# Kernel optimization log

Measured on AMD Instinct MI355X. Metric: run time of the kernel, lower is better.

## Reference

```python
import jax, jax.numpy as jnp
import numpy as np

B, T, C = 2, 2048, 1024
N_HEAD, N_GROUP = 16, 4
N_KV = N_HEAD // N_GROUP          # 4
HEAD_DIM = C // N_HEAD            # 64
ROPE_BASE = 10000.0
INIT_STD = 0.02


def setup_inputs() -> dict:
    key = jax.random.key(0)
    ks = jax.random.split(key, 5)
    kvC = N_KV * HEAD_DIM
    return {
        "x": jax.random.normal(ks[0], (B, T, C), jnp.float32),
        "w_q": jax.random.normal(ks[1], (C, C), jnp.float32) * INIT_STD,
        "b_q": jnp.zeros((C,), jnp.float32),
        "w_k": jax.random.normal(ks[2], (C, kvC), jnp.float32) * INIT_STD,
        "b_k": jnp.zeros((kvC,), jnp.float32),
        "w_v": jax.random.normal(ks[3], (C, kvC), jnp.float32) * INIT_STD,
        "b_v": jnp.zeros((kvC,), jnp.float32),
        "w_o": jax.random.normal(ks[4], (C, C), jnp.float32) * INIT_STD,
        "b_o": jnp.zeros((C,), jnp.float32),
    }


def reference(x, w_q, b_q, w_k, b_k, w_v, b_v, w_o, b_o):
    Bx, Tx, Cx = x.shape
    # projections (torch Linear math with weights stored as [in, out])
    q = (x @ w_q + b_q).reshape(Bx, Tx, N_HEAD, HEAD_DIM).transpose(0, 2, 1, 3)  # [B,H,T,hd]
    k = (x @ w_k + b_k).reshape(Bx, Tx, N_KV, HEAD_DIM).transpose(0, 2, 1, 3)    # [B,KV,T,hd]
    v = (x @ w_v + b_v).reshape(Bx, Tx, N_KV, HEAD_DIM).transpose(0, 2, 1, 3)

    # RoPE with INTERLEAVED pair convention: pairs are (dim 2i, dim 2i+1)
    inv_freq = 1.0 / (ROPE_BASE ** (jnp.arange(0, HEAD_DIM, 2, dtype=jnp.float32) / HEAD_DIM))
    freqs = jnp.arange(Tx, dtype=jnp.float32)[:, None] * inv_freq[None, :]       # [T, hd/2]
    cos, sin = jnp.cos(freqs), jnp.sin(freqs)

    def rope(t):
        tp = t.reshape(*t.shape[:-1], HEAD_DIM // 2, 2)
        e, o = tp[..., 0], tp[..., 1]          # even/odd lanes, [B,h,T,hd/2]
        er = e * cos - o * sin
        orr = e * sin + o * cos
        return jnp.stack([er, orr], axis=-1).reshape(t.shape)

    q, k = rope(q), rope(k)

    # GQA: duplicate each KV head n_group times (consecutively, like repeat_interleave)
    k = jnp.repeat(k, N_GROUP, axis=1)   # [B,H,T,hd]
    v = jnp.repeat(v, N_GROUP, axis=1)

    attn = jnp.einsum('bhqd,bhkd->bhqk', q, k) / np.sqrt(HEAD_DIM).astype(np.float32)
    causal = jnp.tril(jnp.ones((Tx, Tx), bool))
    attn = jnp.where(causal, attn, -jnp.inf)
    attn = jax.nn.softmax(attn, axis=-1)

    out = jnp.einsum('bhqk,bhkd->bhqd', attn, v)            # [B,H,T,hd]
    out = out.transpose(0, 2, 1, 3).reshape(Bx, Tx, Cx)
    return out @ w_o + b_o
```

## Files before the change

### kernel.cpp

```cpp
#include <hip/hip_runtime.h>
#include <hip/hip_bf16.h>

typedef __hip_bfloat16 bf16;
typedef __attribute__((ext_vector_type(8))) short short8_t;
typedef __attribute__((ext_vector_type(4))) short short4_t;
typedef __attribute__((ext_vector_type(4))) float f32x4;

#define B_SZ   2
#define T_SEQ  2048
#define C_DIM  1024
#define NH     16
#define NKV    4
#define HD     64
#define QKVW   1536
#define MTOK   (B_SZ * T_SEQ)

#define LOG2_BASE_OVER_32 0.4152410118609203f
#define Q_SCALE 0.1803368801111204f

__device__ __forceinline__ short f2bs(float f) {
    unsigned u = __float_as_uint(f);
    u += 0x7FFFu + ((u >> 16) & 1u);
    return (short)(u >> 16);
}
__device__ __forceinline__ short f2bs_trunc(float f) {
    return (short)(__float_as_uint(f) >> 16);
}
__device__ __forceinline__ float bs2f(short s) {
    unsigned u = ((unsigned)(unsigned short)s) << 16;
    return __uint_as_float(u);
}
__device__ __forceinline__ float dpp_xor1(float x) {
    return __int_as_float(
        __builtin_amdgcn_update_dpp(0, __float_as_int(x), 0xB1, 0xF, 0xF, true));
}
__device__ __forceinline__ float fast_exp2(float x) {
    float r;
    asm("v_exp_f32 %0, %1" : "=v"(r) : "v"(x));
    return r;
}
__device__ __forceinline__ unsigned pack_bf16_trunc(float lo, float hi) {
    return __builtin_amdgcn_perm(__float_as_uint(hi), __float_as_uint(lo),
                                 0x07060302u);
}
__device__ __forceinline__ void gload_lds16(const short* g, short* l) {
    __builtin_amdgcn_global_load_lds(
        (const __attribute__((address_space(1))) void*)g,
        (__attribute__((address_space(3))) void*)l, 16, 0, 0);
}

__device__ __forceinline__ void transpose_tile(
    const float* __restrict__ W, short* __restrict__ Wt,
    int K, int N, int n0, int k0, int tid)
{
    __shared__ float tile[32][33];
    int tx = tid & 31, ty = tid >> 5;
    #pragma unroll
    for (int i = 0; i < 4; ++i)
        tile[ty + 8 * i][tx] = W[(size_t)(k0 + ty + 8 * i) * N + n0 + tx];
    __syncthreads();
    #pragma unroll
    for (int i = 0; i < 4; ++i)
        Wt[(size_t)(n0 + ty + 8 * i) * K + k0 + tx] = f2bs(tile[tx][ty + 8 * i]);
}

__global__ __launch_bounds__(256) void prep_kernel(
    const float* __restrict__ x,
    const float* __restrict__ w_q, const float* __restrict__ w_k,
    const float* __restrict__ w_v, const float* __restrict__ w_o,
    const float* __restrict__ b_q, const float* __restrict__ b_k,
    const float* __restrict__ b_v,
    short* __restrict__ Xb, short* __restrict__ Wqkv, short* __restrict__ Wto,
    float* __restrict__ Bqkv, float2* __restrict__ Tab)
{
    int blk = blockIdx.x, tid = threadIdx.x;
    if (blk < 4096) {
        int i = blk * 1024 + tid * 4;
        float4 v = *(const float4*)(x + i);
        short4_t o;
        o[0] = f2bs(v.x); o[1] = f2bs(v.y); o[2] = f2bs(v.z); o[3] = f2bs(v.w);
        *(short4_t*)(Xb + i) = o;
    } else if (blk < 5120) {
        int l = blk - 4096;
        transpose_tile(w_q, Wqkv, C_DIM, C_DIM, (l & 31) * 32, (l >> 5) * 32, tid);
    } else if (blk < 5376) {
        int l = blk - 5120;
        transpose_tile(w_k, Wqkv + (size_t)1024 * C_DIM, C_DIM, 256,
                       (l & 7) * 32, (l >> 3) * 32, tid);
    } else if (blk < 5632) {
        int l = blk - 5376;
        transpose_tile(w_v, Wqkv + (size_t)1280 * C_DIM, C_DIM, 256,
                       (l & 7) * 32, (l >> 3) * 32, tid);
    } else if (blk < 6656) {
        int l = blk - 5632;
        transpose_tile(w_o, Wto, C_DIM, C_DIM, (l & 31) * 32, (l >> 5) * 32, tid);
    } else if (blk < 6662) {
        int i = (blk - 6656) * 256 + tid;
        float v;
        if (i < 1024)      v = b_q[i];
        else if (i < 1280) v = b_k[i - 1024];
        else               v = b_v[i - 1280];
        Bqkv[i] = v;
    } else {
        int idx = (blk - 6662) * 256 + tid;
        int t = idx >> 5, i = idx & 31;
        float ang = (float)t * exp2f(-(float)i * LOG2_BASE_OVER_32);
        Tab[idx] = make_float2(cosf(ang), sinf(ang));
    }
}

#define GEMM_STAGE(dstA, dstB, Aptr, Bptr, k0)                                  \
    {                                                                           \
        _Pragma("unroll")                                                       \
        for (int it = 0; it < 4; ++it) {                                        \
            int i = (w * 4 + it) * 64 + lane;                                   \
            int row = i >> 3, p = i & 7;                                        \
            int gc = (k0) + ((p ^ (row & 7)) << 3);                             \
            gload_lds16((Aptr) + (size_t)(m0 + row) * K + gc,                   \
                        (dstA) + (w * 4 + it) * 512);                           \
        }                                                                       \
        _Pragma("unroll")                                                       \
        for (int it = 0; it < 4; ++it) {                                        \
            int i = (w * 4 + it) * 64 + lane;                                   \
            int row = i >> 3, p = i & 7;                                        \
            int gc = (k0) + ((p ^ (row & 7)) << 3);                             \
            gload_lds16((Bptr) + (size_t)(n0 + row) * K + gc,                   \
                        (dstB) + (w * 4 + it) * 512);                           \
        }                                                                       \
    }

#define GEMM_COMPUTE(srcA, srcB)                                                \
    {                                                                           \
        _Pragma("unroll")                                                       \
        for (int ks = 0; ks < 2; ++ks) {                                        \
            short8_t af[4], bf[4];                                              \
            _Pragma("unroll")                                                   \
            for (int mt = 0; mt < 4; ++mt) {                                    \
                int r = wm * 64 + mt * 16 + l16;                                \
                int g = ks * 4 + quad;                                          \
                af[mt] = *(const short8_t*)&(srcA)[r * 64 + ((g ^ (r & 7)) << 3)]; \
            }                                                                   \
            _Pragma("unroll")                                                   \
            for (int nt = 0; nt < 4; ++nt) {                                    \
                int r = wn * 64 + nt * 16 + l16;                                \
                int g = ks * 4 + quad;                                          \
                bf[nt] = *(const short8_t*)&(srcB)[r * 64 + ((g ^ (r & 7)) << 3)]; \
            }                                                                   \
            _Pragma("unroll")                                                   \
            for (int mt = 0; mt < 4; ++mt)                                      \
                _Pragma("unroll")                                               \
                for (int nt = 0; nt < 4; ++nt)                                  \
                    acc[mt][nt] = __builtin_amdgcn_mfma_f32_16x16x32_bf16(      \
                        af[mt], bf[nt], acc[mt][nt], 0, 0, 0);                  \
        }                                                                       \
    }

#define GEMM_KLOOP(Aptr, Bptr)                                                  \
    GEMM_STAGE(sA(0), sB(0), Aptr, Bptr, 0);                                    \
    for (int t = 0; t < NT; ++t) {                                              \
        int cur = t & 1;                                                        \
        if (t + 1 < NT) {                                                       \
            GEMM_STAGE(sA(cur ^ 1), sB(cur ^ 1), Aptr, Bptr, (t + 1) * 64);     \
            asm volatile("s_waitcnt vmcnt(8)" ::: "memory");                    \
        } else {                                                                \
            asm volatile("s_waitcnt vmcnt(0)" ::: "memory");                    \
        }                                                                       \
        __builtin_amdgcn_s_barrier();                                           \
        __builtin_amdgcn_sched_barrier(0);                                      \
        GEMM_COMPUTE(sA(cur), sB(cur));                                         \
        __builtin_amdgcn_sched_barrier(0);                                      \
        __builtin_amdgcn_s_barrier();                                           \
    }

__global__ __launch_bounds__(256) void gemm_qkv(
    const short* __restrict__ A, const short* __restrict__ Bt,
    const float* __restrict__ bias, const float2* __restrict__ Tab,
    short* __restrict__ QKVb, short* __restrict__ Vt)
{
    __shared__ __align__(16) short smem[32768];
    #define sA(b) (smem + (b) * 16384)
    #define sB(b) (smem + (b) * 16384 + 8192)

    const int K = C_DIM, NT = C_DIM / 64;
    int m0 = blockIdx.y * 128;
    int n0 = blockIdx.x * 128;
    int tid  = threadIdx.x;
    int w    = tid >> 6, lane = tid & 63;
    int quad = lane >> 4, l16 = lane & 15;
    int wm = w & 1, wn = w >> 1;

    f32x4 acc[4][4] = {};

    GEMM_KLOOP(A, Bt);

    if (n0 < 1280) {
        float scale = (n0 < 1024) ? Q_SCALE : 1.0f;
        float sgn   = (l16 & 1) ? 1.0f : -1.0f;
        #pragma unroll
        for (int nt = 0; nt < 4; ++nt) {
            int col = n0 + wn * 64 + nt * 16 + l16;
            int ip  = (col & 63) >> 1;
            float bv = bias[col];
            #pragma unroll
            for (int mt = 0; mt < 4; ++mt) {
                #pragma unroll
                for (int r = 0; r < 4; ++r) {
                    int row = m0 + wm * 64 + mt * 16 + quad * 4 + r;
                    float v = acc[mt][nt][r] + bv;
                    float po = dpp_xor1(v);
                    float2 cs = Tab[(row & (T_SEQ - 1)) * 32 + ip];
                    float res = (v * cs.x + sgn * po * cs.y) * scale;
                    QKVb[(size_t)row * QKVW + col] = f2bs(res);
                }
            }
        }
    } else {
        short (*sT)[136] = (short(*)[136])smem;
        #pragma unroll
        for (int h2 = 0; h2 < 2; ++h2) {
            if (wn == h2) {
                #pragma unroll
                for (int nt = 0; nt < 4; ++nt) {
                    int col_l = nt * 16 + l16;
                    float bv = bias[n0 + h2 * 64 + col_l];
                    #pragma unroll
                    for (int mt = 0; mt < 4; ++mt)
                        #pragma unroll
                        for (int r = 0; r < 4; ++r)
                            sT[col_l][wm * 64 + mt * 16 + quad * 4 + r] =
                                f2bs(acc[mt][nt][r] + bv);
                }
            }
            __syncthreads();
            int d0 = n0 - 1280 + h2 * 64;
            #pragma unroll
            for (int it = 0; it < 4; ++it) {
                int slot = tid + 256 * it;
                int dl = slot >> 4, seg = (slot & 15) * 8;
                *(short8_t*)(Vt + (size_t)(d0 + dl) * MTOK + m0 + seg) =
                    *(const short8_t*)&sT[dl][seg];
            }
            __syncthreads();
        }
    }
    #undef sA
    #undef sB
}

__global__ __launch_bounds__(256) void gemm_mfma_o(
    const short* __restrict__ A, const short* __restrict__ Bt,
    const float* __restrict__ bias, float* __restrict__ C,
    int M, int N, int K_, int unused)
{
    __shared__ __align__(16) short smem[32768];
    #define sA(b) (smem + (b) * 16384)
    #define sB(b) (smem + (b) * 16384 + 8192)

    const int K = C_DIM, NT = C_DIM / 64;
    int m0 = blockIdx.y * 128;
    int n0 = blockIdx.x * 128;
    int tid  = threadIdx.x;
    int w    = tid >> 6, lane = tid & 63;
    int quad = lane >> 4, l16 = lane & 15;
    int wm = w & 1, wn = w >> 1;

    f32x4 acc[4][4] = {};

    GEMM_KLOOP(A, Bt);

    #pragma unroll
    for (int mt = 0; mt < 4; ++mt) {
        #pragma unroll
        for (int nt = 0; nt < 4; ++nt) {
            int col = n0 + wn * 64 + nt * 16 + l16;
            float bv = bias[col];
            #pragma unroll
            for (int r = 0; r < 4; ++r) {
                int row = m0 + wm * 64 + mt * 16 + quad * 4 + r;
                C[(size_t)row * N + col] = acc[mt][nt][r] + bv;
            }
        }
    }
    #undef sA
    #undef sB
}

__global__ __launch_bounds__(256) void attn_mfma11(
    const short* __restrict__ QKV, const short* __restrict__ Vt,
    short* __restrict__ O)
{
    __shared__ __align__(16) short sK [2][64][72];
    __shared__ __align__(16) short sVt[2][64][72];

    const int tid  = threadIdx.x;
    const int w    = tid >> 6;
    const int lane = tid & 63;
    const int quad = lane >> 4;
    const int l16  = lane & 15;

    int blk = blockIdx.x;
    int grp = blk & 7;
    int tq  = 127 - (blk >> 3);
    int kvh = grp & 3;
    int b   = grp >> 2;
    int h   = kvh * 4 + w;
    int ct  = tq >> 2;
    int tg  = tq * 16 + l16;

    const short* qptr = QKV + ((size_t)(b * T_SEQ) + tq * 16 + l16) * QKVW + h * HD;
    short8_t qf0 = *(const short8_t*)(qptr + quad * 8);
    short8_t qf1 = *(const short8_t*)(qptr + quad * 8 + 32);

    const short* kbase  = QKV + (size_t)b * T_SEQ * QKVW + 1024 + kvh * HD;
    const short* vtbase = Vt + (size_t)(kvh * HD) * MTOK + b * T_SEQ;

    float m_l = -INFINITY, l_l = 0.f;
    f32x4 oacc[4];
    #pragma unroll
    for (int dt = 0; dt < 4; ++dt) oacc[dt] = (f32x4){0.f, 0.f, 0.f, 0.f};

    const int kkey = tid >> 3, kd = (tid & 7) * 8;
    const int vdim = tid >> 3;
    const int s8   = tid & 7;
    const int vseg = s8 * 8;
    const int P0 = ((s8 & 4) << 3) | ((s8 & 1) << 4) | ((s8 & 2) << 1);

    short8_t kr[2], vr[2];
    #pragma unroll
    for (int it = 0; it < 2; ++it) {
        kr[it] = *(const short8_t*)(kbase + (size_t)(kkey + 32 * it) * QKVW + kd);
        vr[it] = *(const short8_t*)(vtbase + (size_t)(vdim + 32 * it) * MTOK + vseg);
    }

    #pragma unroll
    for (int it = 0; it < 2; ++it) {
        *(short8_t*)&sK[0][kkey + 32 * it][kd] = kr[it];
        union { short8_t v; short4_t h[2]; } u; u.v = vr[it];
        *(short4_t*)&sVt[0][vdim + 32 * it][P0]     = u.h[0];
        *(short4_t*)&sVt[0][vdim + 32 * it][P0 + 8] = u.h[1];
    }
    __syncthreads();

    for (int c = 0; c <= ct; ++c) {
        const int buf = c & 1;

        if (c < ct) {
            int jn = (c + 1) * 64;
            #pragma unroll
            for (int it = 0; it < 2; ++it) {
                kr[it] = *(const short8_t*)(kbase + (size_t)(jn + kkey + 32 * it) * QKVW + kd);
                vr[it] = *(const short8_t*)(vtbase + (size_t)(vdim + 32 * it) * MTOK + jn + vseg);
            }
        }

        f32x4 sacc[4];
        __builtin_amdgcn_s_setprio(1);
        #pragma unroll
        for (int kt = 0; kt < 4; ++kt) {
            f32x4 z = {0.f, 0.f, 0.f, 0.f};
            short8_t kf0 = *(const short8_t*)&sK[buf][l16 + 16 * kt][quad * 8];
            short8_t kf1 = *(const short8_t*)&sK[buf][l16 + 16 * kt][quad * 8 + 32];
            z = __builtin_amdgcn_mfma_f32_16x16x32_bf16(kf0, qf0, z, 0, 0, 0);
            z = __builtin_amdgcn_mfma_f32_16x16x32_bf16(kf1, qf1, z, 0, 0, 0);
            sacc[kt] = z;
        }
        __builtin_amdgcn_s_setprio(0);

        short8_t vf0[4];
        #pragma unroll
        for (int dt = 0; dt < 4; ++dt)
            vf0[dt] = *(const short8_t*)&sVt[buf][16 * dt + l16][quad * 8];

        if (c == ct) {
            int j0 = c * 64;
            #pragma unroll
            for (int kt = 0; kt < 4; ++kt)
                #pragma unroll
                for (int r = 0; r < 4; ++r)
                    if (j0 + 16 * kt + quad * 4 + r > tg) sacc[kt][r] = -INFINITY;
        }

        float v0 = fmaxf(fmaxf(sacc[0][0], sacc[0][1]), fmaxf(sacc[0][2], sacc[0][3]));
        float v1 = fmaxf(fmaxf(sacc[1][0], sacc[1][1]), fmaxf(sacc[1][2], sacc[1][3]));
        float v2 = fmaxf(fmaxf(sacc[2][0], sacc[2][1]), fmaxf(sacc[2][2], sacc[2][3]));
        float v3 = fmaxf(fmaxf(sacc[3][0], sacc[3][1]), fmaxf(sacc[3][2], sacc[3][3]));
        float vloc = fmaxf(fmaxf(v0, v1), fmaxf(v2, v3));

        if (!__all(vloc <= m_l + 8.0f)) {
            float vmax = fmaxf(vloc, __shfl_xor(vloc, 16));
            vmax = fmaxf(vmax, __shfl_xor(vmax, 32));
            float mnew = fmaxf(m_l, vmax);
            float al = fast_exp2(m_l - mnew);
            m_l = mnew;
            l_l *= al;
            #pragma unroll
            for (int r = 0; r < 4; ++r) {
                float alr = __shfl(al, quad * 4 + r);
                #pragma unroll
                for (int dt = 0; dt < 4; ++dt) oacc[dt][r] *= alr;
            }
        }

        float psum = 0.f;
        unsigned pk0, pk1, pk2, pk3, pk4, pk5, pk6, pk7;
        {
            float p0 = fast_exp2(sacc[0][0] - m_l), p1 = fast_exp2(sacc[0][1] - m_l);
            float p2 = fast_exp2(sacc[0][2] - m_l), p3 = fast_exp2(sacc[0][3] - m_l);
            psum += (p0 + p1) + (p2 + p3);
            pk0 = pack_bf16_trunc(p0, p1); pk1 = pack_bf16_trunc(p2, p3);
        }
        {
            float p0 = fast_exp2(sacc[1][0] - m_l), p1 = fast_exp2(sacc[1][1] - m_l);
            float p2 = fast_exp2(sacc[1][2] - m_l), p3 = fast_exp2(sacc[1][3] - m_l);
            psum += (p0 + p1) + (p2 + p3);
            pk2 = pack_bf16_trunc(p0, p1); pk3 = pack_bf16_trunc(p2, p3);
        }
        {
            float p0 = fast_exp2(sacc[2][0] - m_l), p1 = fast_exp2(sacc[2][1] - m_l);
            float p2 = fast_exp2(sacc[2][2] - m_l), p3 = fast_exp2(sacc[2][3] - m_l);
            psum += (p0 + p1) + (p2 + p3);
            pk4 = pack_bf16_trunc(p0, p1); pk5 = pack_bf16_trunc(p2, p3);
        }
        {
            float p0 = fast_exp2(sacc[3][0] - m_l), p1 = fast_exp2(sacc[3][1] - m_l);
            float p2 = fast_exp2(sacc[3][2] - m_l), p3 = fast_exp2(sacc[3][3] - m_l);
            psum += (p0 + p1) + (p2 + p3);
            pk6 = pack_bf16_trunc(p0, p1); pk7 = pack_bf16_trunc(p2, p3);
        }
        l_l += psum;

        short8_t pf0, pf1;
        {
            union { unsigned u[4]; short8_t v; } fa, fb;
            fa.u[0] = pk0; fa.u[1] = pk1; fa.u[2] = pk2; fa.u[3] = pk3;
            fb.u[0] = pk4; fb.u[1] = pk5; fb.u[2] = pk6; fb.u[3] = pk7;
            pf0 = fa.v; pf1 = fb.v;
        }

        __builtin_amdgcn_s_setprio(1);
        #pragma unroll
        for (int dt = 0; dt < 4; ++dt) {
            short8_t vf1 = *(const short8_t*)&sVt[buf][16 * dt + l16][quad * 8 + 32];
            oacc[dt] = __builtin_amdgcn_mfma_f32_16x16x32_bf16(pf0, vf0[dt], oacc[dt], 0, 0, 0);
            oacc[dt] = __builtin_amdgcn_mfma_f32_16x16x32_bf16(pf1, vf1, oacc[dt], 0, 0, 0);
        }
        __builtin_amdgcn_s_setprio(0);

        if (c < ct) {
            #pragma unroll
            for (int it = 0; it < 2; ++it) {
                *(short8_t*)&sK[buf ^ 1][kkey + 32 * it][kd] = kr[it];
                union { short8_t v; short4_t h[2]; } u; u.v = vr[it];
                *(short4_t*)&sVt[buf ^ 1][vdim + 32 * it][P0]     = u.h[0];
                *(short4_t*)&sVt[buf ^ 1][vdim + 32 * it][P0 + 8] = u.h[1];
            }
        }
        __syncthreads();
    }

    l_l += __shfl_xor(l_l, 16);
    l_l += __shfl_xor(l_l, 32);

    #pragma unroll
    for (int r = 0; r < 4; ++r) {
        int m = quad * 4 + r;
        float lr = __shfl(l_l, quad * 4 + r);
        float inv = __builtin_amdgcn_rcpf(lr);
        #pragma unroll
        for (int dt = 0; dt < 4; ++dt)
            O[((size_t)b * T_SEQ + tq * 16 + m) * C_DIM + h * HD + 16 * dt + l16] =
                f2bs(oacc[dt][r] * inv);
    }
}

extern "C" void kernel_launch(void* const* d_in, const int* in_sizes, int n_in,
                              void* d_out, int out_size, void* d_ws, size_t ws_size,
                              hipStream_t stream)
{
    const float* x   = (const float*)d_in[0];
    const float* w_q = (const float*)d_in[1];
    const float* b_q = (const float*)d_in[2];
    const float* w_k = (const float*)d_in[3];
    const float* b_k = (const float*)d_in[4];
    const float* w_v = (const float*)d_in[5];
    const float* b_v = (const float*)d_in[6];
    const float* w_o = (const float*)d_in[7];
    const float* b_o = (const float*)d_in[8];
    float* out = (float*)d_out;

    char* ws = (char*)d_ws;
    short*  Xb   = (short*) (ws);
    short*  Ab   = (short*) (ws + ((size_t)8  << 20));
    short*  QKVb = (short*) (ws + ((size_t)16 << 20));
    short*  Wqkv = (short*) (ws + ((size_t)28 << 20));
    short*  Wto  = (short*) (ws + ((size_t)31 << 20));
    float*  Bqkv = (float*) (ws + ((size_t)33 << 20));
    float2* Tab  = (float2*)(ws + ((size_t)33 << 20) + 8192);
    short*  Vt   = (short*) (ws + ((size_t)34 << 20));

    const int M = MTOK;

    prep_kernel<<<6918, 256, 0, stream>>>(
        x, w_q, w_k, w_v, w_o, b_q, b_k, b_v, Xb, Wqkv, Wto, Bqkv, Tab);

    gemm_qkv<<<dim3(QKVW / 128, M / 128), 256, 0, stream>>>(
        Xb, Wqkv, Bqkv, Tab, QKVb, Vt);

    attn_mfma11<<<B_SZ * NKV * 128, 256, 0, stream>>>(QKVb, Vt, Ab);

    gemm_mfma_o<<<dim3(C_DIM / 128, M / 128), 256, 0, stream>>>(
        Ab, Wto, b_o, out, M, C_DIM, C_DIM, 0);
}
```

Baseline: 164.6 us.

## Share K/V tiles across two query tiles per 512-thread attention block

The attention kernel now runs 512 threads (8 waves) per block, covering two adjacent 16-row query tiles for the four heads of a KV group. Each loaded K/V tile is therefore reused by twice as many waves, and the grid is halved. K is moved into LDS with direct global-to-LDS loads (gload_lds16) into an XOR-swizzled, unpadded layout, replacing the register staging. Risks are lower occupancy from the larger blocks, more waves waiting at each barrier, and the first wave pair doing a wasted causal half-tile on the diagonal chunk.

```diff
diff --git a/kernel.cpp b/kernel.cpp
--- a/kernel.cpp
+++ b/kernel.cpp
@@ -285,11 +285,11 @@
     #undef sB
 }
 
-__global__ __launch_bounds__(256) void attn_mfma11(
+__global__ __launch_bounds__(512) void attn_mfma14(
     const short* __restrict__ QKV, const short* __restrict__ Vt,
     short* __restrict__ O)
 {
-    __shared__ __align__(16) short sK [2][64][72];
+    __shared__ __align__(16) short sK [2][64][64];
     __shared__ __align__(16) short sVt[2][64][72];
 
     const int tid  = threadIdx.x;
@@ -300,11 +300,12 @@
 
     int blk = blockIdx.x;
     int grp = blk & 7;
-    int tq  = 127 - (blk >> 3);
+    int pr  = 63 - (blk >> 3);
     int kvh = grp & 3;
     int b   = grp >> 2;
-    int h   = kvh * 4 + w;
-    int ct  = tq >> 2;
+    int h   = kvh * 4 + (w & 3);
+    int tq  = pr * 2 + (w >> 2);
+    int ct  = pr >> 1;
     int tg  = tq * 16 + l16;
 
     const short* qptr = QKV + ((size_t)(b * T_SEQ) + tq * 16 + l16) * QKVW + h * HD;
@@ -319,38 +320,35 @@
     #pragma unroll
     for (int dt = 0; dt < 4; ++dt) oacc[dt] = (f32x4){0.f, 0.f, 0.f, 0.f};
 
-    const int kkey = tid >> 3, kd = (tid & 7) * 8;
+    const int kr_  = tid >> 3;
+    const int kg   = tid & 7;
+    const int ksrc = (kg ^ (kr_ & 7)) << 3;
+
     const int vdim = tid >> 3;
     const int s8   = tid & 7;
     const int vseg = s8 * 8;
-    const int P0 = ((s8 & 4) << 3) | ((s8 & 1) << 4) | ((s8 & 2) << 1);
-
-    short8_t kr[2], vr[2];
-    #pragma unroll
-    for (int it = 0; it < 2; ++it) {
-        kr[it] = *(const short8_t*)(kbase + (size_t)(kkey + 32 * it) * QKVW + kd);
-        vr[it] = *(const short8_t*)(vtbase + (size_t)(vdim + 32 * it) * MTOK + vseg);
-    }
-
-    #pragma unroll
-    for (int it = 0; it < 2; ++it) {
-        *(short8_t*)&sK[0][kkey + 32 * it][kd] = kr[it];
-        union { short8_t v; short4_t h[2]; } u; u.v = vr[it];
-        *(short4_t*)&sVt[0][vdim + 32 * it][P0]     = u.h[0];
-        *(short4_t*)&sVt[0][vdim + 32 * it][P0 + 8] = u.h[1];
+    const int P0   = ((s8 & 4) << 3) | ((s8 & 1) << 4) | ((s8 & 2) << 1);
+
+    const int c0g = quad ^ (l16 & 7);
+
+    gload_lds16(kbase + (size_t)kr_ * QKVW + ksrc, (short*)sK[0] + (w << 9));
+    {
+        short8_t v0 = *(const short8_t*)(vtbase + (size_t)vdim * MTOK + vseg);
+        union { short8_t v; short4_t h[2]; } u; u.v = v0;
+        *(short4_t*)&sVt[0][vdim][P0]     = u.h[0];
+        *(short4_t*)&sVt[0][vdim][P0 + 8] = u.h[1];
     }
     __syncthreads();
 
+    short8_t vr;
     for (int c = 0; c <= ct; ++c) {
         const int buf = c & 1;
 
         if (c < ct) {
             int jn = (c + 1) * 64;
-            #pragma unroll
-            for (int it = 0; it < 2; ++it) {
-                kr[it] = *(const short8_t*)(kbase + (size_t)(jn + kkey + 32 * it) * QKVW + kd);
-                vr[it] = *(const short8_t*)(vtbase + (size_t)(vdim + 32 * it) * MTOK + jn + vseg);
-            }
+            gload_lds16(kbase + (size_t)(jn + kr_) * QKVW + ksrc,
+                        (short*)sK[buf ^ 1] + (w << 9));
+            vr = *(const short8_t*)(vtbase + (size_t)vdim * MTOK + jn + vseg);
         }
 
         f32x4 sacc[4];
@@ -358,8 +356,9 @@
         #pragma unroll
         for (int kt = 0; kt < 4; ++kt) {
             f32x4 z = {0.f, 0.f, 0.f, 0.f};
-            short8_t kf0 = *(const short8_t*)&sK[buf][l16 + 16 * kt][quad * 8];
-            short8_t kf1 = *(const short8_t*)&sK[buf][l16 + 16 * kt][quad * 8 + 32];
+            const short* krow = &sK[buf][l16 + 16 * kt][0];
+            short8_t kf0 = *(const short8_t*)(krow + (c0g << 3));
+            short8_t kf1 = *(const short8_t*)(krow + ((c0g ^ 4) << 3));
             z = __builtin_amdgcn_mfma_f32_16x16x32_bf16(kf0, qf0, z, 0, 0, 0);
             z = __builtin_amdgcn_mfma_f32_16x16x32_bf16(kf1, qf1, z, 0, 0, 0);
             sacc[kt] = z;
@@ -447,13 +446,9 @@
         __builtin_amdgcn_s_setprio(0);
 
         if (c < ct) {
-            #pragma unroll
-            for (int it = 0; it < 2; ++it) {
-                *(short8_t*)&sK[buf ^ 1][kkey + 32 * it][kd] = kr[it];
-                union { short8_t v; short4_t h[2]; } u; u.v = vr[it];
-                *(short4_t*)&sVt[buf ^ 1][vdim + 32 * it][P0]     = u.h[0];
-                *(short4_t*)&sVt[buf ^ 1][vdim + 32 * it][P0 + 8] = u.h[1];
-            }
+            union { short8_t v; short4_t h[2]; } u; u.v = vr;
+            *(short4_t*)&sVt[buf ^ 1][vdim][P0]     = u.h[0];
+            *(short4_t*)&sVt[buf ^ 1][vdim][P0 + 8] = u.h[1];
         }
         __syncthreads();
     }
@@ -506,7 +501,7 @@
     gemm_qkv<<<dim3(QKVW / 128, M / 128), 256, 0, stream>>>(
         Xb, Wqkv, Bqkv, Tab, QKVb, Vt);
 
-    attn_mfma11<<<B_SZ * NKV * 128, 256, 0, stream>>>(QKVb, Vt, Ab);
+    attn_mfma14<<<B_SZ * NKV * 64, 512, 0, stream>>>(QKVb, Vt, Ab);
 
     gemm_mfma_o<<<dim3(C_DIM / 128, M / 128), 256, 0, stream>>>(
         Ab, Wto, b_o, out, M, C_DIM, C_DIM, 0);
```

Measured after the change: 162.7 us. Within noise of the previous version (-1.2%).
